# Kernel tuning notes

Hardware: AMD Instinct MI355X
Metric: run time of the kernel (lower is better)

## Reference

```python
import jax, jax.numpy as jnp
import numpy as np

N = 50000
E = 1600000
T = 9
F_IN = 128
H = 128
OUT = 32


def setup_inputs() -> dict:
    key = jax.random.key(0)
    ks = jax.random.split(key, 10)
    s = 0.05
    return {
        "x_seq": jax.random.normal(ks[0], (T, N, F_IN), dtype=jnp.float32),
        "edge_index": jax.random.randint(ks[1], (2, E), 0, N, dtype=jnp.int64),
        "W_gcn": jax.random.normal(ks[2], (F_IN, H), dtype=jnp.float32) * s,
        "b_gcn": jnp.zeros((H,), jnp.float32),
        "W_ih": jax.random.normal(ks[3], (4 * H, H), dtype=jnp.float32) * s,
        "W_hh": jax.random.normal(ks[4], (4 * H, H), dtype=jnp.float32) * s,
        "b_ih": jnp.zeros((4 * H,), jnp.float32),
        "b_hh": jnp.zeros((4 * H,), jnp.float32),
        "W_fc": jax.random.normal(ks[5], (OUT, H), dtype=jnp.float32) * s,
        "b_fc": jnp.zeros((OUT,), jnp.float32),
    }


def reference(x_seq, edge_index, W_gcn, b_gcn, W_ih, W_hh, b_ih, b_hh, W_fc, b_fc):
    # eval mode: all dropouts are identity (F.dropout training=False, 1-layer LSTM dropout is a no-op)
    t_steps, n, _ = x_seq.shape
    h_dim = W_hh.shape[1]
    loops = jnp.arange(n)
    row = jnp.concatenate([edge_index[0], loops])  # sources (with self loops)
    col = jnp.concatenate([edge_index[1], loops])  # targets
    deg = jax.ops.segment_sum(jnp.ones_like(row, dtype=x_seq.dtype), col, num_segments=n)
    dinv = jax.lax.rsqrt(deg)
    norm = (dinv[row] * dinv[col])[:, None]  # [E+N, 1]

    def gcn(x_t):
        h = x_t @ W_gcn                                          # [N, H]
        agg = jax.ops.segment_sum(h[row] * norm, col, num_segments=n)
        return jax.nn.relu(agg + b_gcn)

    # small fixed loop over T=9 to avoid materializing [T, E, H] messages at once
    emb = jnp.stack([gcn(x_seq[t]) for t in range(t_steps)], axis=0)  # [T, N, H]

    def step(carry, x_t):
        h, c = carry
        gates = x_t @ W_ih.T + h @ W_hh.T + b_ih + b_hh
        i, f, g, o = jnp.split(gates, 4, axis=-1)  # torch LSTM gate order: i, f, g, o
        c = jax.nn.sigmoid(f) * c + jax.nn.sigmoid(i) * jnp.tanh(g)
        h = jax.nn.sigmoid(o) * jnp.tanh(c)
        return (h, c), h

    h0 = jnp.zeros((n, h_dim), x_seq.dtype)
    _, hs = jax.lax.scan(step, (h0, h0), emb)      # [T, N, H]
    lstm_out = jnp.transpose(hs, (1, 0, 2))        # batch_first: [N, T, H]
    return lstm_out @ W_fc.T + b_fc                # [N, T, OUT]
```

## Files before the change

### kernel.cpp

```cpp
#include <hip/hip_runtime.h>
#include <cstdint>
#include <cstddef>


constexpr int N    = 50000;
constexpr int NP   = 50048;
constexpr int E    = 1600000;
constexpr int T    = 9;
constexpr int H    = 128;
constexpr int G    = 512;
constexpr int OUTD = 32;

constexpr int SCAN_CH = 512;
constexpr int NCH = (N + SCAN_CH - 1) / SCAN_CH;

constexpr int GNWG = (NP / 128) * 4;
constexpr int GQQ  = GNWG / 8;
constexpr int GRR  = GNWG % 8;

typedef __attribute__((ext_vector_type(8))) _Float16 f16x8;
typedef __attribute__((ext_vector_type(4))) float f32x4;
typedef __attribute__((ext_vector_type(4))) _Float16 f16x4;

__device__ __forceinline__ void gll16(const void* g, void* l) {
  __builtin_amdgcn_global_load_lds(
      (const __attribute__((address_space(1))) void*)g,
      (__attribute__((address_space(3))) void*)l, 16, 0, 0);
}


__global__ void k_count(const int* __restrict__ col, int* __restrict__ cnt) {
  int e = blockIdx.x * 256 + threadIdx.x;
  if (e < E) atomicAdd(&cnt[col[e]], 1);
}

__global__ void k_dinv(const int* __restrict__ cnt, float* __restrict__ dinv) {
  int v = blockIdx.x * 256 + threadIdx.x;
  if (v < N) dinv[v] = rsqrtf((float)cnt[v] + 1.0f);
}

__global__ void k_chunk_sum(const int* __restrict__ cnt, int* __restrict__ csum) {
  __shared__ int sp[SCAN_CH / 64];
  int i = blockIdx.x * SCAN_CH + threadIdx.x;
  int v = (i < N) ? cnt[i] : 0;
  for (int off = 32; off > 0; off >>= 1) v += __shfl_down(v, off, 64);
  if ((threadIdx.x & 63) == 0) sp[threadIdx.x >> 6] = v;
  __syncthreads();
  if (threadIdx.x == 0) {
    int s = 0;
    #pragma unroll
    for (int w = 0; w < SCAN_CH / 64; ++w) s += sp[w];
    csum[blockIdx.x] = s;
  }
}

__global__ void k_chunk_scan(const int* __restrict__ csum, int* __restrict__ coff) {
  if (blockIdx.x == 0 && threadIdx.x == 0) {
    int run = 0;
    for (int b = 0; b < NCH; ++b) { coff[b] = run; run += csum[b]; }
    coff[NCH] = run;
  }
}

__global__ void k_scan_final(const int* __restrict__ cnt, const int* __restrict__ coff,
                             int* __restrict__ offv) {
  __shared__ int s[SCAN_CH];
  int tid = threadIdx.x;
  int i = blockIdx.x * SCAN_CH + tid;
  int v = (i < N) ? cnt[i] : 0;
  s[tid] = v;
  __syncthreads();
  for (int st = 1; st < SCAN_CH; st <<= 1) {
    int tv = (tid >= st) ? s[tid - st] : 0;
    __syncthreads();
    s[tid] += tv;
    __syncthreads();
  }
  if (i < N) offv[i] = coff[blockIdx.x] + s[tid] - v;
  if (blockIdx.x == 0 && tid == 0) offv[N] = coff[NCH];
}

__global__ void k_fill(const int* __restrict__ row, const int* __restrict__ col,
                       const float* __restrict__ dinv, const int* __restrict__ offv,
                       int* __restrict__ cursor, int2* __restrict__ csr) {
  int e = blockIdx.x * 256 + threadIdx.x;
  if (e >= E) return;
  int r = row[e], c = col[e];
  int p = atomicAdd(&cursor[c], 1);
  float nm = dinv[r] * dinv[c];
  csr[offv[c] + p] = make_int2(r, __builtin_bit_cast(int, nm));
}

__global__ void k_wprep_lstm(const float* __restrict__ Wih, const float* __restrict__ Whh,
                             _Float16* __restrict__ bt) {
  int idx = blockIdx.x * 256 + threadIdx.x;
  if (idx >= G * 256) return;
  int j = idx >> 8, k = idx & 255;
  float f = (k < H) ? Wih[j * H + k] : Whh[j * H + (k - H)];
  bt[idx] = (_Float16)f;
}

__global__ void k_wprep_gcn(const float* __restrict__ Wg, _Float16* __restrict__ bgT) {
  int idx = blockIdx.x * 256 + threadIdx.x;
  if (idx >= H * H) return;
  int j = idx >> 7, k = idx & 127;
  bgT[idx] = (_Float16)Wg[k * H + j];
}

__global__ void k_wprep_fc(const float* __restrict__ Wfc, _Float16* __restrict__ w16) {
  int idx = blockIdx.x * 256 + threadIdx.x;
  if (idx < OUTD * H) w16[idx] = (_Float16)Wfc[idx];
}

__global__ __launch_bounds__(256) void k_gcn_all(const float* __restrict__ Xall,
                                                 const _Float16* __restrict__ BgT,
                                                 _Float16* __restrict__ xw_all) {
  __shared__ _Float16 lsB[16384];
  const float* X = Xall + (size_t)blockIdx.y * N * H;
  _Float16* xw = xw_all + (size_t)blockIdx.y * H;
  int tid = threadIdx.x;
  int lane = tid & 63, wid = tid >> 6;
  int wr = wid >> 1, wc = wid & 1;
  int rb = blockIdx.x * 128 + wr * 64;
  int cb = wc * 64;
  int lr = lane & 15;
  int g  = lane >> 4;

  #pragma unroll
  for (int i = 0; i < 8; ++i) {
    int c = i * 256 + tid;
    int kb = c >> 9, j = (c >> 2) & 127, gg = c & 3;
    f16x8 v = *(const f16x8*)&BgT[j * H + kb * 32 + gg * 8];
    int slot = gg ^ ((j >> 1) & 3);
    *(f16x8*)&lsB[kb * 4096 + j * 32 + slot * 8] = v;
  }
  __syncthreads();

  f32x4 acc[4][4];
  #pragma unroll
  for (int mi = 0; mi < 4; ++mi)
    #pragma unroll
    for (int ni = 0; ni < 4; ++ni) acc[mi][ni] = (f32x4)0.0f;

  #pragma unroll
  for (int kb = 0; kb < 4; ++kb) {
    f16x8 bfr[4];
    #pragma unroll
    for (int ni = 0; ni < 4; ++ni) {
      int j = cb + ni * 16 + lr;
      bfr[ni] = *(const f16x8*)&lsB[kb * 4096 + j * 32 + (g ^ ((j >> 1) & 3)) * 8];
    }
    #pragma unroll
    for (int mi = 0; mi < 4; ++mi) {
      int r = rb + mi * 16 + lr;
      r = r < N ? r : N - 1;
      const float* ap = X + (size_t)r * H + kb * 32 + g * 8;
      float4 a0 = *(const float4*)ap;
      float4 a1 = *(const float4*)(ap + 4);
      f16x8 afr;
      afr[0] = (_Float16)a0.x; afr[1] = (_Float16)a0.y;
      afr[2] = (_Float16)a0.z; afr[3] = (_Float16)a0.w;
      afr[4] = (_Float16)a1.x; afr[5] = (_Float16)a1.y;
      afr[6] = (_Float16)a1.z; afr[7] = (_Float16)a1.w;
      #pragma unroll
      for (int ni = 0; ni < 4; ++ni)
        acc[mi][ni] = __builtin_amdgcn_mfma_f32_16x16x32_f16(afr, bfr[ni], acc[mi][ni], 0, 0, 0);
    }
  }
  int orow = (lane >> 4) * 4;
  #pragma unroll
  for (int mi = 0; mi < 4; ++mi)
    #pragma unroll
    for (int ni = 0; ni < 4; ++ni)
      #pragma unroll
      for (int r = 0; r < 4; ++r) {
        int n = rb + mi * 16 + orow + r;
        if (n < N) xw[(size_t)n * (T * H) + cb + ni * 16 + lr] = (_Float16)acc[mi][ni][r];
      }
}

__global__ __launch_bounds__(256) void k_agg_all(const _Float16* __restrict__ xw_all,
                                                 const int* __restrict__ offv,
                                                 const long long* __restrict__ csr,
                                                 const float* __restrict__ dinv,
                                                 const float* __restrict__ bg,
                                                 _Float16* __restrict__ emb_all) {
  int wid = threadIdx.x >> 6, lane = threadIdx.x & 63;
  int v = blockIdx.x * 4 + wid;
  int half = lane >> 5, sl = lane & 31;
  int c0 = sl * 4;
  float acc[T][4];
  #pragma unroll
  for (int t = 0; t < T; ++t) {
    acc[t][0] = 0.f; acc[t][1] = 0.f; acc[t][2] = 0.f; acc[t][3] = 0.f;
  }
  if (half == 0) {
    float dv = dinv[v];
    float w = dv * dv;
    const _Float16* xp = xw_all + (size_t)v * (T * H) + c0;
    #pragma unroll
    for (int t = 0; t < T; ++t) {
      f16x4 xs = *(const f16x4*)(xp + t * H);
      acc[t][0] = (float)xs.x * w; acc[t][1] = (float)xs.y * w;
      acc[t][2] = (float)xs.z * w; acc[t][3] = (float)xs.w * w;
    }
  }
  int e0 = offv[v], e1 = offv[v + 1];
  for (int e = e0 + half; e < e1; e += 2) {
    long long raw = __builtin_nontemporal_load(&csr[e]);
    int s = (int)(raw & 0xffffffffLL);
    float m = __builtin_bit_cast(float, (int)(raw >> 32));
    const _Float16* xp = xw_all + (size_t)s * (T * H) + c0;
    #pragma unroll
    for (int t = 0; t < T; ++t) {
      f16x4 x = *(const f16x4*)(xp + t * H);
      acc[t][0] = fmaf((float)x.x, m, acc[t][0]);
      acc[t][1] = fmaf((float)x.y, m, acc[t][1]);
      acc[t][2] = fmaf((float)x.z, m, acc[t][2]);
      acc[t][3] = fmaf((float)x.w, m, acc[t][3]);
    }
  }
  #pragma unroll
  for (int t = 0; t < T; ++t) {
    acc[t][0] += __shfl_xor(acc[t][0], 32, 64);
    acc[t][1] += __shfl_xor(acc[t][1], 32, 64);
    acc[t][2] += __shfl_xor(acc[t][2], 32, 64);
    acc[t][3] += __shfl_xor(acc[t][3], 32, 64);
  }
  if (half == 0) {
    float4 bb = *(const float4*)&bg[c0];
    #pragma unroll
    for (int t = 0; t < T; ++t) {
      f16x4 ov;
      ov.x = (_Float16)fmaxf(acc[t][0] + bb.x, 0.f);
      ov.y = (_Float16)fmaxf(acc[t][1] + bb.y, 0.f);
      ov.z = (_Float16)fmaxf(acc[t][2] + bb.z, 0.f);
      ov.w = (_Float16)fmaxf(acc[t][3] + bb.w, 0.f);
      __builtin_nontemporal_store(ov,
          (f16x4*)&emb_all[(size_t)t * N * H + (size_t)v * H + c0]);
    }
  }
}

template<bool FIRST>
__global__ __launch_bounds__(256) void k_gates_cell(const _Float16* __restrict__ embt,
                                                    const _Float16* __restrict__ hcur,
                                                    const _Float16* __restrict__ Bt,
                                                    const float* __restrict__ bih,
                                                    const float* __restrict__ bhh,
                                                    float* __restrict__ cbuf,
                                                    _Float16* __restrict__ oH) {
  __shared__ _Float16 ls[2][8192];
  const int tid = threadIdx.x;
  const int lane = tid & 63, wid = tid >> 6;
  const int wr = wid >> 1, wc = wid & 1;
  const int lr = lane & 15;
  const int g  = lane >> 4;

  int xcd = blockIdx.x & 7, loc = blockIdx.x >> 3;
  int wgid = (xcd < GRR ? xcd * (GQQ + 1) : GRR * (GQQ + 1) + (xcd - GRR) * GQQ) + loc;
  const int rb  = (wgid >> 2) * 128;
  const int ch0 = (wgid & 3) * 32;

  f32x4 acc[4][4];
  #pragma unroll
  for (int mi = 0; mi < 4; ++mi)
    #pragma unroll
    for (int ni = 0; ni < 4; ++ni) acc[mi][ni] = (f32x4)0.0f;

  auto stage = [&](int buf, int kb) {
    const _Float16* srcA = (kb < 4) ? embt : hcur;
    int koA = (kb & 3) * 32;
    int koB = kb * 32;
    _Float16* lb = &ls[buf][0];
    #pragma unroll
    for (int i = 0; i < 2; ++i) {
      int c = i * 256 + tid;
      int row = c >> 2, slot = c & 3;
      int g3 = slot ^ ((row >> 1) & 3);
      size_t ga = (size_t)(rb + row) * H + koA + g3 * 8;
      gll16(srcA + ga, lb + c * 8);
      int j = (row >> 5) * 128 + ch0 + (row & 31);
      size_t gb = (size_t)j * 256 + koB + g3 * 8;
      gll16(Bt + gb, lb + 4096 + c * 8);
    }
  };

  auto compute = [&](int buf) {
    const _Float16* lb = &ls[buf][0];
    f16x8 bfr[4];
    #pragma unroll
    for (int ni = 0; ni < 4; ++ni) {
      int jj = ni * 32 + wc * 16 + lr;
      bfr[ni] = *(const f16x8*)(lb + 4096 + jj * 32 + (g ^ ((jj >> 1) & 3)) * 8);
    }
    #pragma unroll
    for (int mi = 0; mi < 4; ++mi) {
      int rr = wr * 64 + mi * 16 + lr;
      f16x8 afr = *(const f16x8*)(lb + rr * 32 + (g ^ ((rr >> 1) & 3)) * 8);
      #pragma unroll
      for (int ni = 0; ni < 4; ++ni)
        acc[mi][ni] = __builtin_amdgcn_mfma_f32_16x16x32_f16(afr, bfr[ni], acc[mi][ni], 0, 0, 0);
    }
  };

  const int kbs = FIRST ? 4 : 8;
  stage(0, 0);
  for (int kb = 0; kb < kbs; ++kb) {
    __syncthreads();
    if (kb + 1 < kbs) stage((kb + 1) & 1, kb + 1);
    compute(kb & 1);
  }

  int ch = ch0 + wc * 16 + lr;
  float bi_ = bih[ch]       + bhh[ch];
  float bf_ = bih[128 + ch] + bhh[128 + ch];
  float bg_ = bih[256 + ch] + bhh[256 + ch];
  float bo_ = bih[384 + ch] + bhh[384 + ch];
  int orow = (lane >> 4) * 4;
  int rbw = rb + wr * 64;
  #pragma unroll
  for (int mi = 0; mi < 4; ++mi) {
    #pragma unroll
    for (int r = 0; r < 4; ++r) {
      int n = rbw + mi * 16 + orow + r;
      if (n >= N) continue;
      float gi = acc[mi][0][r] + bi_;
      float gf = acc[mi][1][r] + bf_;
      float gg = acc[mi][2][r] + bg_;
      float go = acc[mi][3][r] + bo_;
      float si = 1.f / (1.f + expf(-gi));
      float sf = 1.f / (1.f + expf(-gf));
      float so = 1.f / (1.f + expf(-go));
      float tg = tanhf(gg);
      size_t ci = (size_t)n * H + ch;
      float cn = FIRST ? si * tg : fmaf(sf, cbuf[ci], si * tg);
      cbuf[ci] = cn;
      float hn = so * tanhf(cn);
      oH[ci] = (_Float16)hn;
    }
  }
}

__global__ __launch_bounds__(256) void k_fc_mfma(const _Float16* __restrict__ Hc,
                                                 const _Float16* __restrict__ w16,
                                                 const float* __restrict__ bfc,
                                                 float* __restrict__ outp, int t) {
  int lane = threadIdx.x & 63, wid = threadIdx.x >> 6;
  int rb = blockIdx.x * 256 + wid * 64;
  int lr = lane & 15, g = lane >> 4;
  f32x4 acc[4][2];
  #pragma unroll
  for (int mi = 0; mi < 4; ++mi) { acc[mi][0] = (f32x4)0.0f; acc[mi][1] = (f32x4)0.0f; }

  #pragma unroll
  for (int kb = 0; kb < 4; ++kb) {
    int ko = kb * 32 + g * 8;
    f16x8 bfr[2];
    #pragma unroll
    for (int ni = 0; ni < 2; ++ni)
      bfr[ni] = *(const f16x8*)&w16[(ni * 16 + lr) * H + ko];
    #pragma unroll
    for (int mi = 0; mi < 4; ++mi) {
      int n = rb + mi * 16 + lr;
      n = n < N ? n : N - 1;
      f16x8 afr = *(const f16x8*)&Hc[(size_t)n * H + ko];
      #pragma unroll
      for (int ni = 0; ni < 2; ++ni)
        acc[mi][ni] = __builtin_amdgcn_mfma_f32_16x16x32_f16(afr, bfr[ni], acc[mi][ni], 0, 0, 0);
    }
  }
  int orow = g * 4;
  #pragma unroll
  for (int ni = 0; ni < 2; ++ni) {
    int oc = ni * 16 + lr;
    float bb = bfc[oc];
    #pragma unroll
    for (int mi = 0; mi < 4; ++mi)
      #pragma unroll
      for (int r = 0; r < 4; ++r) {
        int n = rb + mi * 16 + orow + r;
        if (n < N) outp[((size_t)n * T + t) * OUTD + oc] = acc[mi][ni][r] + bb;
      }
  }
}


extern "C" void kernel_launch(void* const* d_in, const int* in_sizes, int n_in,
                              void* d_out, int out_size, void* d_ws, size_t ws_size,
                              hipStream_t stream) {
  const float* x_seq = (const float*)d_in[0];
  const int*   eidx  = (const int*)d_in[1];
  const int*   erow  = eidx;
  const int*   ecol  = eidx + E;
  const float* W_gcn = (const float*)d_in[2];
  const float* b_gcn = (const float*)d_in[3];
  const float* W_ih  = (const float*)d_in[4];
  const float* W_hh  = (const float*)d_in[5];
  const float* b_ih  = (const float*)d_in[6];
  const float* b_hh  = (const float*)d_in[7];
  const float* W_fc  = (const float*)d_in[8];
  const float* b_fc  = (const float*)d_in[9];
  float* outp = (float*)d_out;

  char* base = (char*)d_ws;
  size_t o = 0;
  auto alloc = [&](size_t bytes) -> void* {
    void* p = base + o;
    o += (bytes + 255) & ~(size_t)255;
    return p;
  };
  int*   cnt      = (int*)  alloc((size_t)N * 4);
  int*   cursor   = (int*)  alloc((size_t)N * 4);
  int*   offv     = (int*)  alloc((size_t)(N + 1) * 4);
  int*   csum     = (int*)  alloc((size_t)(NCH + 1) * 4);
  int*   coff     = (int*)  alloc((size_t)(NCH + 1) * 4);
  float* dinv     = (float*)alloc((size_t)N * 4);
  int2*  csr      = (int2*) alloc((size_t)E * 8);
  _Float16* bt    = (_Float16*)alloc((size_t)G * 256 * 2);
  _Float16* bgT   = (_Float16*)alloc((size_t)H * H * 2);
  _Float16* wfc16 = (_Float16*)alloc((size_t)OUTD * H * 2);
  _Float16* xw_all = (_Float16*)alloc((size_t)N * T * H * 2);
  _Float16* emb_all= (_Float16*)alloc((size_t)(T * N + 128) * H * 2);
  _Float16* h0    = (_Float16*)alloc((size_t)NP * H * 2);
  _Float16* h1    = (_Float16*)alloc((size_t)NP * H * 2);
  float* cbuf     = (float*)alloc((size_t)N * H * 4);
  (void)ws_size; (void)in_sizes; (void)n_in; (void)out_size;

  _Float16* HP[2] = {h0, h1};

  hipMemsetAsync(cnt,    0, (size_t)N * 4, stream);
  hipMemsetAsync(cursor, 0, (size_t)N * 4, stream);

  k_count<<<E / 256, 256, 0, stream>>>(ecol, cnt);
  k_dinv<<<(N + 255) / 256, 256, 0, stream>>>(cnt, dinv);
  k_chunk_sum<<<NCH, SCAN_CH, 0, stream>>>(cnt, csum);
  k_chunk_scan<<<1, 64, 0, stream>>>(csum, coff);
  k_scan_final<<<NCH, SCAN_CH, 0, stream>>>(cnt, coff, offv);
  k_fill<<<E / 256, 256, 0, stream>>>(erow, ecol, dinv, offv, cursor, csr);
  k_wprep_lstm<<<(G * 256) / 256, 256, 0, stream>>>(W_ih, W_hh, bt);
  k_wprep_gcn<<<(H * H) / 256, 256, 0, stream>>>(W_gcn, bgT);
  k_wprep_fc<<<(OUTD * H + 255) / 256, 256, 0, stream>>>(W_fc, wfc16);

  k_gcn_all<<<dim3(NP / 128, T), 256, 0, stream>>>(x_seq, bgT, xw_all);
  k_agg_all<<<N / 4, 256, 0, stream>>>(xw_all, offv, (const long long*)csr,
                                       dinv, b_gcn, emb_all);

  int fcblocks = (NP + 255) / 256;
  for (int t = 0; t < T; ++t) {
    int cur = t & 1, nxt = cur ^ 1;
    const _Float16* embt = emb_all + (size_t)t * N * H;
    if (t == 0)
      k_gates_cell<true><<<GNWG, 256, 0, stream>>>(
          embt, HP[cur], bt, b_ih, b_hh, cbuf, HP[nxt]);
    else
      k_gates_cell<false><<<GNWG, 256, 0, stream>>>(
          embt, HP[cur], bt, b_ih, b_hh, cbuf, HP[nxt]);
    k_fc_mfma<<<fcblocks, 256, 0, stream>>>(HP[nxt], wfc16, b_fc, outp, t);
  }
}
```

Baseline: 1.260 ms.

## Split GCN aggregation into two time chunks with smaller gather footprint

The projected features are split into two buffers holding 5 and 4 timesteps each, and aggregation runs as two passes. The aim is to shrink the per-pass gather working set (about 64MB and 51MB instead of 115MB) so it fits better in the last-level cache. The edge loop is also unrolled by two so each lane keeps more independent gathers in flight. In exchange the CSR and offsets are read twice and there is one more launch.

```diff
diff --git a/kernel.cpp b/kernel.cpp
--- a/kernel.cpp
+++ b/kernel.cpp
@@ -10,6 +10,8 @@
 constexpr int H    = 128;
 constexpr int G    = 512;
 constexpr int OUTD = 32;
+constexpr int TCA  = 5;
+constexpr int TCB  = 4;
 
 constexpr int SCAN_CH = 512;
 constexpr int NCH = (N + SCAN_CH - 1) / SCAN_CH;
@@ -114,10 +116,15 @@
 
 __global__ __launch_bounds__(256) void k_gcn_all(const float* __restrict__ Xall,
                                                  const _Float16* __restrict__ BgT,
-                                                 _Float16* __restrict__ xw_all) {
+                                                 _Float16* __restrict__ xwA,
+                                                 _Float16* __restrict__ xwB) {
   __shared__ _Float16 lsB[16384];
-  const float* X = Xall + (size_t)blockIdx.y * N * H;
-  _Float16* xw = xw_all + (size_t)blockIdx.y * H;
+  int t = blockIdx.y;
+  const float* X = Xall + (size_t)t * N * H;
+  _Float16* xw;
+  int rs;
+  if (t < TCA) { xw = xwA + t * H;         rs = TCA * H; }
+  else         { xw = xwB + (t - TCA) * H; rs = TCB * H; }
   int tid = threadIdx.x;
   int lane = tid & 63, wid = tid >> 6;
   int wr = wid >> 1, wc = wid & 1;
@@ -175,53 +182,83 @@
       #pragma unroll
       for (int r = 0; r < 4; ++r) {
         int n = rb + mi * 16 + orow + r;
-        if (n < N) xw[(size_t)n * (T * H) + cb + ni * 16 + lr] = (_Float16)acc[mi][ni][r];
+        if (n < N) xw[(size_t)n * rs + cb + ni * 16 + lr] = (_Float16)acc[mi][ni][r];
       }
 }
 
-__global__ __launch_bounds__(256) void k_agg_all(const _Float16* __restrict__ xw_all,
-                                                 const int* __restrict__ offv,
-                                                 const long long* __restrict__ csr,
-                                                 const float* __restrict__ dinv,
-                                                 const float* __restrict__ bg,
-                                                 _Float16* __restrict__ emb_all) {
+template<int TC>
+__global__ __launch_bounds__(256) void k_agg_chunk(const _Float16* __restrict__ xw,
+                                                   const int* __restrict__ offv,
+                                                   const long long* __restrict__ csr,
+                                                   const float* __restrict__ dinv,
+                                                   const float* __restrict__ bg,
+                                                   _Float16* __restrict__ embc) {
+  constexpr int RS = TC * H;
   int wid = threadIdx.x >> 6, lane = threadIdx.x & 63;
   int v = blockIdx.x * 4 + wid;
   int half = lane >> 5, sl = lane & 31;
   int c0 = sl * 4;
-  float acc[T][4];
-  #pragma unroll
-  for (int t = 0; t < T; ++t) {
+  float acc[TC][4];
+  #pragma unroll
+  for (int t = 0; t < TC; ++t) {
     acc[t][0] = 0.f; acc[t][1] = 0.f; acc[t][2] = 0.f; acc[t][3] = 0.f;
   }
   if (half == 0) {
     float dv = dinv[v];
     float w = dv * dv;
-    const _Float16* xp = xw_all + (size_t)v * (T * H) + c0;
-    #pragma unroll
-    for (int t = 0; t < T; ++t) {
+    const _Float16* xp = xw + (size_t)v * RS + c0;
+    #pragma unroll
+    for (int t = 0; t < TC; ++t) {
       f16x4 xs = *(const f16x4*)(xp + t * H);
       acc[t][0] = (float)xs.x * w; acc[t][1] = (float)xs.y * w;
       acc[t][2] = (float)xs.z * w; acc[t][3] = (float)xs.w * w;
     }
   }
   int e0 = offv[v], e1 = offv[v + 1];
-  for (int e = e0 + half; e < e1; e += 2) {
-    long long raw = __builtin_nontemporal_load(&csr[e]);
-    int s = (int)(raw & 0xffffffffLL);
-    float m = __builtin_bit_cast(float, (int)(raw >> 32));
-    const _Float16* xp = xw_all + (size_t)s * (T * H) + c0;
-    #pragma unroll
-    for (int t = 0; t < T; ++t) {
-      f16x4 x = *(const f16x4*)(xp + t * H);
-      acc[t][0] = fmaf((float)x.x, m, acc[t][0]);
-      acc[t][1] = fmaf((float)x.y, m, acc[t][1]);
-      acc[t][2] = fmaf((float)x.z, m, acc[t][2]);
-      acc[t][3] = fmaf((float)x.w, m, acc[t][3]);
-    }
-  }
-  #pragma unroll
-  for (int t = 0; t < T; ++t) {
+  int e = e0 + half;
+  for (; e + 2 < e1; e += 4) {
+    long long r0 = __builtin_nontemporal_load(&csr[e]);
+    long long r1 = __builtin_nontemporal_load(&csr[e + 2]);
+    int s0 = (int)(r0 & 0xffffffffLL);
+    int s1 = (int)(r1 & 0xffffffffLL);
+    float m0 = __builtin_bit_cast(float, (int)(r0 >> 32));
+    float m1 = __builtin_bit_cast(float, (int)(r1 >> 32));
+    const _Float16* xp0 = xw + (size_t)s0 * RS + c0;
+    const _Float16* xp1 = xw + (size_t)s1 * RS + c0;
+    f16x4 xa[TC], xb[TC];
+    #pragma unroll
+    for (int t = 0; t < TC; ++t) {
+      xa[t] = *(const f16x4*)(xp0 + t * H);
+      xb[t] = *(const f16x4*)(xp1 + t * H);
+    }
+    #pragma unroll
+    for (int t = 0; t < TC; ++t) {
+      acc[t][0] = fmaf((float)xa[t].x, m0, acc[t][0]);
+      acc[t][1] = fmaf((float)xa[t].y, m0, acc[t][1]);
+      acc[t][2] = fmaf((float)xa[t].z, m0, acc[t][2]);
+      acc[t][3] = fmaf((float)xa[t].w, m0, acc[t][3]);
+      acc[t][0] = fmaf((float)xb[t].x, m1, acc[t][0]);
+      acc[t][1] = fmaf((float)xb[t].y, m1, acc[t][1]);
+      acc[t][2] = fmaf((float)xb[t].z, m1, acc[t][2]);
+      acc[t][3] = fmaf((float)xb[t].w, m1, acc[t][3]);
+    }
+  }
+  if (e < e1) {
+    long long r0 = __builtin_nontemporal_load(&csr[e]);
+    int s0 = (int)(r0 & 0xffffffffLL);
+    float m0 = __builtin_bit_cast(float, (int)(r0 >> 32));
+    const _Float16* xp0 = xw + (size_t)s0 * RS + c0;
+    #pragma unroll
+    for (int t = 0; t < TC; ++t) {
+      f16x4 x = *(const f16x4*)(xp0 + t * H);
+      acc[t][0] = fmaf((float)x.x, m0, acc[t][0]);
+      acc[t][1] = fmaf((float)x.y, m0, acc[t][1]);
+      acc[t][2] = fmaf((float)x.z, m0, acc[t][2]);
+      acc[t][3] = fmaf((float)x.w, m0, acc[t][3]);
+    }
+  }
+  #pragma unroll
+  for (int t = 0; t < TC; ++t) {
     acc[t][0] += __shfl_xor(acc[t][0], 32, 64);
     acc[t][1] += __shfl_xor(acc[t][1], 32, 64);
     acc[t][2] += __shfl_xor(acc[t][2], 32, 64);
@@ -230,14 +267,14 @@
   if (half == 0) {
     float4 bb = *(const float4*)&bg[c0];
     #pragma unroll
-    for (int t = 0; t < T; ++t) {
+    for (int t = 0; t < TC; ++t) {
       f16x4 ov;
       ov.x = (_Float16)fmaxf(acc[t][0] + bb.x, 0.f);
       ov.y = (_Float16)fmaxf(acc[t][1] + bb.y, 0.f);
       ov.z = (_Float16)fmaxf(acc[t][2] + bb.z, 0.f);
       ov.w = (_Float16)fmaxf(acc[t][3] + bb.w, 0.f);
       __builtin_nontemporal_store(ov,
-          (f16x4*)&emb_all[(size_t)t * N * H + (size_t)v * H + c0]);
+          (f16x4*)&embc[(size_t)t * N * H + (size_t)v * H + c0]);
     }
   }
 }
@@ -420,7 +457,8 @@
   _Float16* bt    = (_Float16*)alloc((size_t)G * 256 * 2);
   _Float16* bgT   = (_Float16*)alloc((size_t)H * H * 2);
   _Float16* wfc16 = (_Float16*)alloc((size_t)OUTD * H * 2);
-  _Float16* xw_all = (_Float16*)alloc((size_t)N * T * H * 2);
+  _Float16* xwA   = (_Float16*)alloc((size_t)N * TCA * H * 2);
+  _Float16* xwB   = (_Float16*)alloc((size_t)N * TCB * H * 2);
   _Float16* emb_all= (_Float16*)alloc((size_t)(T * N + 128) * H * 2);
   _Float16* h0    = (_Float16*)alloc((size_t)NP * H * 2);
   _Float16* h1    = (_Float16*)alloc((size_t)NP * H * 2);
@@ -442,9 +480,12 @@
   k_wprep_gcn<<<(H * H) / 256, 256, 0, stream>>>(W_gcn, bgT);
   k_wprep_fc<<<(OUTD * H + 255) / 256, 256, 0, stream>>>(W_fc, wfc16);
 
-  k_gcn_all<<<dim3(NP / 128, T), 256, 0, stream>>>(x_seq, bgT, xw_all);
-  k_agg_all<<<N / 4, 256, 0, stream>>>(xw_all, offv, (const long long*)csr,
-                                       dinv, b_gcn, emb_all);
+  k_gcn_all<<<dim3(NP / 128, T), 256, 0, stream>>>(x_seq, bgT, xwA, xwB);
+  k_agg_chunk<TCA><<<N / 4, 256, 0, stream>>>(xwA, offv, (const long long*)csr,
+                                              dinv, b_gcn, emb_all);
+  k_agg_chunk<TCB><<<N / 4, 256, 0, stream>>>(xwB, offv, (const long long*)csr,
+                                              dinv, b_gcn,
+                                              emb_all + (size_t)TCA * N * H);
 
   int fcblocks = (NP + 255) / 256;
   for (int t = 0; t < T; ++t) {
```

New measurement: 1.255 ms. No clear change (-0.4%).
